# Kernel tuning notes

Measured on AMD Instinct MI355X. Metric: run time of the kernel, lower is better.

Reference implementation:

```python
import jax, jax.numpy as jnp
import numpy as np

B, Wd, C, H, F = 48, 88, 256, 32, 1024
NH_SELF, NH_CROSS = 8, 8


def _ln(x, g, b, eps=1e-5):
    mu = x.mean(-1, keepdims=True)
    var = ((x - mu) ** 2).mean(-1, keepdims=True)
    return (x - mu) / jnp.sqrt(var + eps) * g + b


def setup_inputs() -> dict:
    key = jax.random.key(0)
    ks = jax.random.split(key, 16)
    s = 0.02  # weight init scale
    d = {
        'pooled_features': jax.random.normal(ks[0], (B, Wd, C), jnp.float32),
        'features': jax.random.normal(ks[1], (B, C, H, Wd), jnp.float32),
        'self_pe': jax.random.normal(ks[2], (Wd, C), jnp.float32),
        'cross_pe': jax.random.normal(ks[3], (H, C), jnp.float32),
    }
    # LayerNorm params
    for n in ['ln_qs', 'ln_vs', 'ln_qc', 'ln_kv', 'ln_vc', 'ln_ffn']:
        d[n + '_g'] = jnp.ones((C,), jnp.float32)
        d[n + '_b'] = jnp.zeros((C,), jnp.float32)
    # attention projections (stored [in,out]; y = x @ W + b)
    names = ['Wq_s', 'Wk_s', 'Wv_s', 'Wp_s', 'Wq_c', 'Wk_c', 'Wv_c', 'Wp_c']
    for i, n in enumerate(names):
        d[n] = jax.random.normal(ks[4 + i], (C, C), jnp.float32) * s
    for n in ['bq_s', 'bv_s', 'bp_s', 'bq_c', 'bv_c', 'bp_c']:
        d[n] = jnp.zeros((C,), jnp.float32)
    # FFN
    d['W1'] = jax.random.normal(ks[12], (C, F), jnp.float32) * s
    d['b1'] = jnp.zeros((F,), jnp.float32)
    d['W2'] = jax.random.normal(ks[13], (F, C), jnp.float32) * s
    d['b2'] = jnp.zeros((C,), jnp.float32)
    return d


def reference(pooled_features, features, self_pe, cross_pe,
              ln_qs_g, ln_qs_b, ln_vs_g, ln_vs_b,
              ln_qc_g, ln_qc_b, ln_kv_g, ln_kv_b, ln_vc_g, ln_vc_b,
              ln_ffn_g, ln_ffn_b,
              Wq_s, bq_s, Wk_s, Wv_s, bv_s, Wp_s, bp_s,
              Wq_c, bq_c, Wk_c, Wv_c, bv_c, Wp_c, bp_c,
              W1, b1, W2, b2):
    b, w, c = pooled_features.shape
    h = features.shape[2]
    ds = c // NH_SELF
    dc = c // NH_CROSS

    # ---- cross attention first (op_order='cross_first', with_pe=True) ----
    xq = pooled_features                                  # [B,W,C]
    qn = _ln(xq, ln_qc_g, ln_qc_b)
    kv = jnp.transpose(features, (0, 3, 2, 1))            # [B,W,H,C]
    kn = _ln(kv + cross_pe[None, None], ln_kv_g, ln_kv_b)
    vn = _ln(kv, ln_vc_g, ln_vc_b)
    q = (qn @ Wq_c + bq_c).reshape(b, w, NH_CROSS, dc)    # query len 1 per column
    k = (kn @ Wk_c).reshape(b, w, h, NH_CROSS, dc)
    v = (vn @ Wv_c + bv_c).reshape(b, w, h, NH_CROSS, dc)
    attn = jnp.einsum('bwhd,bwkhd->bwhk', q, k) * (dc ** -0.5)
    attn = jax.nn.softmax(attn, axis=-1)
    out = jnp.einsum('bwhk,bwkhd->bwhd', attn, v).reshape(b, w, c)
    x = out @ Wp_c + bp_c + xq

    # ---- self attention over width tokens ----
    qn = _ln(x + self_pe[None], ln_qs_g, ln_qs_b)
    vn = _ln(x, ln_vs_g, ln_vs_b)
    q = (qn @ Wq_s + bq_s).reshape(b, w, NH_SELF, ds)
    k = (qn @ Wk_s).reshape(b, w, NH_SELF, ds)
    v = (vn @ Wv_s + bv_s).reshape(b, w, NH_SELF, ds)
    attn = jnp.einsum('bnhd,bmhd->bhnm', q, k) * (ds ** -0.5)
    attn = jax.nn.softmax(attn, axis=-1)
    out = jnp.einsum('bhnm,bmhd->bnhd', attn, v).reshape(b, w, c)
    x = out @ Wp_s + bp_s + x

    # ---- FFN (mmcv FFN, num_fcs=2, GELU, identity residual) ----
    hdn = _ln(x, ln_ffn_g, ln_ffn_b)
    hdn = jax.nn.gelu(hdn @ W1 + b1, approximate=False) @ W2 + b2
    return x + hdn
```

## Files before the change

kernel.cpp:

```cpp
#include <hip/hip_runtime.h>
#include <math.h>

#define B_   48
#define W_   88
#define C_   256
#define H_   32
#define F_   1024
#define BW_  (B_ * W_)
#define BWH_ (B_ * W_ * H_)
#define HW_  (H_ * W_)

typedef float  f32x4  __attribute__((ext_vector_type(4)));
typedef __bf16 bf16x8 __attribute__((ext_vector_type(8)));

__device__ __forceinline__ unsigned short f2bf(float f) {
  union { float f; unsigned int u; } v; v.f = f;
  unsigned int r = v.u + 0x7FFFu + ((v.u >> 16) & 1u);
  return (unsigned short)(r >> 16);
}
__device__ __forceinline__ float bf2f(unsigned short h) {
  union { unsigned int u; float f; } v; v.u = ((unsigned int)h) << 16;
  return v.f;
}
__device__ __forceinline__ unsigned int pack2(float a, float b) {
  return (unsigned int)f2bf(a) | ((unsigned int)f2bf(b) << 16);
}

__global__ __launch_bounds__(256) void prep_all(
    const float* __restrict__ Wq_s, const float* __restrict__ Wk_s,
    const float* __restrict__ Wv_s, const float* __restrict__ Wp_s,
    const float* __restrict__ W1, const float* __restrict__ W2,
    const float* __restrict__ Wq_c, const float* __restrict__ Wk_c,
    const float* __restrict__ Wv_c, const float* __restrict__ Wp_c,
    const float* __restrict__ bq_s, const float* __restrict__ bv_s,
    const float* __restrict__ bq_c, const float* __restrict__ bv_c,
    const float* __restrict__ bp_c,
    const float* __restrict__ pooled,
    const float* __restrict__ ln_qc_g, const float* __restrict__ ln_qc_b,
    unsigned short* __restrict__ wqkvs, unsigned short* __restrict__ wps,
    unsigned short* __restrict__ w1t, unsigned short* __restrict__ w2t,
    unsigned short* __restrict__ mqk, unsigned short* __restrict__ mvp,
    float* __restrict__ bqk, float* __restrict__ bvp,
    float* __restrict__ bqkvs, unsigned short* __restrict__ qn_c) {
  __shared__ float smem[256 * 33 + 4 * 33];
  int blk = blockIdx.x, t = threadIdx.x;

  if (blk < 768) {
    const float* src; unsigned short* dst; int Cc, R, tile;
    if (blk < 64)       { src = Wq_s; dst = wqkvs;          Cc = 256;  R = 256;  tile = blk; }
    else if (blk < 128) { src = Wk_s; dst = wqkvs + 65536;  Cc = 256;  R = 256;  tile = blk - 64; }
    else if (blk < 192) { src = Wv_s; dst = wqkvs + 131072; Cc = 256;  R = 256;  tile = blk - 128; }
    else if (blk < 256) { src = Wp_s; dst = wps;            Cc = 256;  R = 256;  tile = blk - 192; }
    else if (blk < 512) { src = W1;   dst = w1t;            Cc = 1024; R = 256;  tile = blk - 256; }
    else                { src = W2;   dst = w2t;            Cc = 256;  R = 1024; tile = blk - 512; }
    int tcn = Cc >> 5;
    int tr = tile / tcn, tc = tile % tcn;
    float (*lds)[33] = (float(*)[33])smem;
    int r = t >> 3, c4 = (t & 7) * 4;
    float4 v = *(const float4*)(src + (size_t)(tr * 32 + r) * Cc + tc * 32 + c4);
    lds[r][c4 + 0] = v.x; lds[r][c4 + 1] = v.y; lds[r][c4 + 2] = v.z; lds[r][c4 + 3] = v.w;
    __syncthreads();
    int rd = t >> 3, cd4 = (t & 7) * 4;
    unsigned int u0 = pack2(lds[cd4 + 0][rd], lds[cd4 + 1][rd]);
    unsigned int u1 = pack2(lds[cd4 + 2][rd], lds[cd4 + 3][rd]);
    uint2 u; u.x = u0; u.y = u1;
    *(uint2*)(dst + (size_t)(tc * 32 + rd) * R + tr * 32 + cd4) = u;
  } else if (blk < 1280) {
    int lb = blk - 768;
    int h = lb >> 6, cb = lb & 63;
    float (*wq)[33] = (float(*)[33])smem;
    float (*wk)[33] = (float(*)[33])(smem + 256 * 33);
#pragma unroll
    for (int p = 0; p < 8; p++) {
      int dp = (t >> 3) + 32 * p, d4 = (t & 7) * 4;
      float4 v = *(const float4*)(Wq_c + (size_t)dp * 256 + 32 * h + d4);
      wq[dp][d4 + 0] = v.x; wq[dp][d4 + 1] = v.y; wq[dp][d4 + 2] = v.z; wq[dp][d4 + 3] = v.w;
    }
    if (t < 128) {
      int c_l = t >> 5, dd = t & 31;
      wk[c_l][dd] = Wk_c[(size_t)(cb * 4 + c_l) * 256 + 32 * h + dd];
    }
    __syncthreads();
    const float scale = 0.17677669529663689f;
    int c_l = t >> 6, ln = t & 63;
    int n = 256 * h + cb * 4 + c_l;
#pragma unroll
    for (int j = 0; j < 4; j++) {
      int dp = ln + 64 * j;
      float acc = 0.f;
#pragma unroll
      for (int dd = 0; dd < 32; dd++) acc += wq[dp][dd] * wk[c_l][dd];
      mqk[(size_t)n * 256 + dp] = f2bf(acc * scale);
    }
    if (ln == 0) {
      float bb = 0.f;
#pragma unroll
      for (int dd = 0; dd < 32; dd++) bb += bq_c[32 * h + dd] * wk[c_l][dd];
      bqk[n] = bb * scale;
    }
  } else if (blk < 1792) {
    int lb = blk - 1280;
    int h = lb >> 6, db = lb & 63;
    float (*wv)[33] = (float(*)[33])smem;
    float (*wp)[33] = (float(*)[33])(smem + 256 * 33);
#pragma unroll
    for (int p = 0; p < 8; p++) {
      int c = (t >> 3) + 32 * p, d4 = (t & 7) * 4;
      float4 v = *(const float4*)(Wv_c + (size_t)c * 256 + 32 * h + d4);
      wv[c][d4 + 0] = v.x; wv[c][d4 + 1] = v.y; wv[c][d4 + 2] = v.z; wv[c][d4 + 3] = v.w;
    }
    if (t < 128) {
      int d_l = t >> 5, dd = t & 31;
      wp[d_l][dd] = Wp_c[(size_t)(32 * h + dd) * 256 + db * 4 + d_l];
    }
    __syncthreads();
    int d_l = t >> 6, ln = t & 63;
    int d = db * 4 + d_l;
#pragma unroll
    for (int j = 0; j < 4; j++) {
      int c = ln + 64 * j;
      float acc = 0.f;
#pragma unroll
      for (int dd = 0; dd < 32; dd++) acc += wv[c][dd] * wp[d_l][dd];
      mvp[(size_t)d * 2048 + 256 * h + c] = f2bf(acc);
    }
  } else if (blk == 1792) {
    float acc = bp_c[t];
    for (int dp = 0; dp < 256; dp++) acc += bv_c[dp] * Wp_c[(size_t)dp * 256 + t];
    bvp[t] = acc;
    bqkvs[t] = bq_s[t]; bqkvs[256 + t] = 0.f; bqkvs[512 + t] = bv_s[t];
  } else {
    int row = blk - 1793, c = t;
    float v = pooled[(size_t)row * C_ + c];
    float s1 = v, s2 = v * v;
#pragma unroll
    for (int m = 32; m > 0; m >>= 1) {
      s1 += __shfl_xor(s1, m, 64); s2 += __shfl_xor(s2, m, 64);
    }
    float* red = smem;
    int wave = c >> 6;
    if ((c & 63) == 0) { red[wave] = s1; red[4 + wave] = s2; }
    __syncthreads();
    s1 = red[0] + red[1] + red[2] + red[3];
    s2 = red[4] + red[5] + red[6] + red[7];
    float mu = s1 * (1.f / C_);
    float rs = rsqrtf(s2 * (1.f / C_) - mu * mu + 1e-5f);
    qn_c[(size_t)row * C_ + c] = f2bf((v - mu) * rs * ln_qc_g[c] + ln_qc_b[c]);
  }
}

__global__ __launch_bounds__(256) void ln_transpose4(
    const float* __restrict__ features, const float* __restrict__ cross_pe,
    const float* __restrict__ g_kv, const float* __restrict__ b_kv,
    const float* __restrict__ g_vc, const float* __restrict__ b_vc,
    unsigned short* __restrict__ kn, unsigned short* __restrict__ vn) {
  int b   = blockIdx.x / 176;
  int tl  = blockIdx.x % 176;
  int hw0 = tl * 16;
  __shared__ float tileT[256][17];
  int t = threadIdx.x;
  {
    int a  = (t & 3) * 4;
    int cc = t >> 2;
    const float* fb = features + (size_t)b * C_ * HW_ + hw0;
#pragma unroll
    for (int p = 0; p < 4; p++) {
      int c = cc + p * 64;
      float4 v = *(const float4*)(fb + (size_t)c * HW_ + a);
      tileT[c][a + 0] = v.x; tileT[c][a + 1] = v.y;
      tileT[c][a + 2] = v.z; tileT[c][a + 3] = v.w;
    }
  }
  __syncthreads();
  int row = t >> 4, ln = t & 15;
  int hw = hw0 + row;
  int hh = hw / 88, ww = hw - hh * 88;
  const float* per = cross_pe + hh * 256;
  float vreg[16], preg[16];
  float s1 = 0, s2 = 0, p1 = 0, p2 = 0;
#pragma unroll
  for (int j = 0; j < 4; j++) {
    int c0 = 4 * ln + 64 * j;
    float4 pv = *(const float4*)(per + c0);
    float pa[4] = {pv.x, pv.y, pv.z, pv.w};
#pragma unroll
    for (int i = 0; i < 4; i++) {
      float v  = tileT[c0 + i][row];
      float vp = v + pa[i];
      vreg[4 * j + i] = v; preg[4 * j + i] = pa[i];
      s1 += v;  s2 += v * v;
      p1 += vp; p2 += vp * vp;
    }
  }
#pragma unroll
  for (int m = 1; m < 16; m <<= 1) {
    s1 += __shfl_xor(s1, m, 16); s2 += __shfl_xor(s2, m, 16);
    p1 += __shfl_xor(p1, m, 16); p2 += __shfl_xor(p2, m, 16);
  }
  float mu  = s1 * (1.f / 256.f);
  float rs  = rsqrtf(s2 * (1.f / 256.f) - mu * mu + 1e-5f);
  float muk = p1 * (1.f / 256.f);
  float rsk = rsqrtf(p2 * (1.f / 256.f) - muk * muk + 1e-5f);
  size_t ro = ((size_t)b * 88 + ww) * 32 + hh;
  unsigned short* vrow = vn + ro * 256;
  unsigned short* krow = kn + ro * 256;
#pragma unroll
  for (int j = 0; j < 4; j++) {
    int c0 = 4 * ln + 64 * j;
    float4 gv = *(const float4*)(g_vc + c0);
    float4 bv = *(const float4*)(b_vc + c0);
    float4 gk = *(const float4*)(g_kv + c0);
    float4 bk = *(const float4*)(b_kv + c0);
    float gva[4] = {gv.x, gv.y, gv.z, gv.w}, bva[4] = {bv.x, bv.y, bv.z, bv.w};
    float gka[4] = {gk.x, gk.y, gk.z, gk.w}, bka[4] = {bk.x, bk.y, bk.z, bk.w};
    float ov[4], ok[4];
#pragma unroll
    for (int i = 0; i < 4; i++) {
      float v = vreg[4 * j + i], p = preg[4 * j + i];
      ov[i] = (v - mu) * rs * gva[i] + bva[i];
      ok[i] = (v + p - muk) * rsk * gka[i] + bka[i];
    }
    uint2 uv, uk;
    uv.x = pack2(ov[0], ov[1]); uv.y = pack2(ov[2], ov[3]);
    uk.x = pack2(ok[0], ok[1]); uk.y = pack2(ok[2], ok[3]);
    *(uint2*)(vrow + c0) = uv;
    *(uint2*)(krow + c0) = uk;
  }
}

__global__ __launch_bounds__(256) void ln_rows(
    const float* __restrict__ x,
    const float* __restrict__ g, const float* __restrict__ bta,
    unsigned short* __restrict__ out) {
  int row = blockIdx.x, c = threadIdx.x;
  float v = x[(size_t)row * C_ + c];
  float s1 = v, s2 = v * v;
#pragma unroll
  for (int m = 32; m > 0; m >>= 1) {
    s1 += __shfl_xor(s1, m, 64);
    s2 += __shfl_xor(s2, m, 64);
  }
  __shared__ float red[8];
  int wave = c >> 6;
  if ((c & 63) == 0) { red[wave] = s1; red[4 + wave] = s2; }
  __syncthreads();
  s1 = red[0] + red[1] + red[2] + red[3];
  s2 = red[4] + red[5] + red[6] + red[7];
  float mu = s1 * (1.f / C_);
  float rs = rsqrtf(s2 * (1.f / C_) - mu * mu + 1e-5f);
  out[(size_t)row * C_ + c] = f2bf((v - mu) * rs * g[c] + bta[c]);
}

__global__ __launch_bounds__(256) void ln_dual(
    const float* __restrict__ x, const float* __restrict__ pe,
    const float* __restrict__ g1, const float* __restrict__ b1a,
    const float* __restrict__ g2, const float* __restrict__ b2a,
    unsigned short* __restrict__ out1, unsigned short* __restrict__ out2) {
  int row = blockIdx.x, c = threadIdx.x;
  float v = x[(size_t)row * C_ + c];
  float vp = v + pe[(size_t)(row % 88) * C_ + c];
  float s1 = v, s2 = v * v, t1 = vp, t2 = vp * vp;
#pragma unroll
  for (int m = 32; m > 0; m >>= 1) {
    s1 += __shfl_xor(s1, m, 64); s2 += __shfl_xor(s2, m, 64);
    t1 += __shfl_xor(t1, m, 64); t2 += __shfl_xor(t2, m, 64);
  }
  __shared__ float red[16];
  int wave = c >> 6;
  if ((c & 63) == 0) {
    red[wave] = s1; red[4 + wave] = s2; red[8 + wave] = t1; red[12 + wave] = t2;
  }
  __syncthreads();
  s1 = red[0] + red[1] + red[2] + red[3];
  s2 = red[4] + red[5] + red[6] + red[7];
  t1 = red[8] + red[9] + red[10] + red[11];
  t2 = red[12] + red[13] + red[14] + red[15];
  float mu = s1 * (1.f / C_), rs = rsqrtf(s2 * (1.f / C_) - mu * mu + 1e-5f);
  float mup = t1 * (1.f / C_), rsp = rsqrtf(t2 * (1.f / C_) - mup * mup + 1e-5f);
  out1[(size_t)row * C_ + c] = f2bf((vp - mup) * rsp * g1[c] + b1a[c]);
  out2[(size_t)row * C_ + c] = f2bf((v - mu) * rs * g2[c] + b2a[c]);
}

__global__ __launch_bounds__(256) void gemm_bt(
    const unsigned short* __restrict__ A, const unsigned short* __restrict__ Bt,
    int M, int N, int K,
    const float* __restrict__ bias, const float* __restrict__ resid,
    float* __restrict__ outF, unsigned short* __restrict__ outB, int act_gelu) {
  __shared__ __attribute__((aligned(16))) unsigned short As[64][32];
  __shared__ __attribute__((aligned(16))) unsigned short Bs[64][32];
  const int tiles_n = N >> 6;
  const int bm = blockIdx.x / tiles_n;
  const int bn = blockIdx.x % tiles_n;
  const int tid = threadIdx.x;
  const int wave = tid >> 6, lane = tid & 63;
  const int quad = lane >> 4, lr = lane & 15;
  const int wm = (wave >> 1) << 5, wn = (wave & 1) << 5;
  const int lrow = tid >> 2;
  const int lcol = (tid & 3) << 3;
  const size_t a_base = (size_t)(bm * 64 + lrow) * K + lcol;
  const size_t b_base = (size_t)(bn * 64 + lrow) * K + lcol;
  f32x4 acc[2][2] = {};
  uint4 areg = *(const uint4*)(A + a_base);
  uint4 breg = *(const uint4*)(Bt + b_base);
  for (int k0 = 0; k0 < K; k0 += 32) {
    *(uint4*)&As[lrow][lcol] = areg;
    *(uint4*)&Bs[lrow][lcol] = breg;
    __syncthreads();
    if (k0 + 32 < K) {
      areg = *(const uint4*)(A + a_base + k0 + 32);
      breg = *(const uint4*)(Bt + b_base + k0 + 32);
    }
    bf16x8 af0 = *(const bf16x8*)&As[wm + lr][quad << 3];
    bf16x8 af1 = *(const bf16x8*)&As[wm + 16 + lr][quad << 3];
    bf16x8 bf0 = *(const bf16x8*)&Bs[wn + lr][quad << 3];
    bf16x8 bf1 = *(const bf16x8*)&Bs[wn + 16 + lr][quad << 3];
    acc[0][0] = __builtin_amdgcn_mfma_f32_16x16x32_bf16(af0, bf0, acc[0][0], 0, 0, 0);
    acc[0][1] = __builtin_amdgcn_mfma_f32_16x16x32_bf16(af0, bf1, acc[0][1], 0, 0, 0);
    acc[1][0] = __builtin_amdgcn_mfma_f32_16x16x32_bf16(af1, bf0, acc[1][0], 0, 0, 0);
    acc[1][1] = __builtin_amdgcn_mfma_f32_16x16x32_bf16(af1, bf1, acc[1][1], 0, 0, 0);
    __syncthreads();
  }
#pragma unroll
  for (int i = 0; i < 2; i++)
#pragma unroll
    for (int j = 0; j < 2; j++)
#pragma unroll
      for (int rr = 0; rr < 4; rr++) {
        int row = bm * 64 + wm + i * 16 + quad * 4 + rr;
        int col = bn * 64 + wn + j * 16 + lr;
        float val = acc[i][j][rr];
        if (bias) val += bias[col];
        if (act_gelu) val = 0.5f * val * (1.f + erff(val * 0.70710678118654752f));
        if (resid) val += resid[(size_t)row * N + col];
        if (outF) outF[(size_t)row * N + col] = val;
        else outB[(size_t)row * N + col] = f2bf(val);
      }
}

__global__ __launch_bounds__(256) void gemm_bt_st(
    const unsigned short* __restrict__ A, const unsigned short* __restrict__ Bt,
    int M, int N, int K, int ldc,
    const float* __restrict__ bias, float* __restrict__ outF) {
  __shared__ __attribute__((aligned(16))) unsigned short As[64][32];
  __shared__ __attribute__((aligned(16))) unsigned short Bs[64][32];
  const int tiles_n = N >> 6;
  const int bm = blockIdx.x / tiles_n;
  const int bn = blockIdx.x % tiles_n;
  const int tid = threadIdx.x;
  const int wave = tid >> 6, lane = tid & 63;
  const int quad = lane >> 4, lr = lane & 15;
  const int wm = (wave >> 1) << 5, wn = (wave & 1) << 5;
  const int lrow = tid >> 2;
  const int lcol = (tid & 3) << 3;
  const size_t a_base = (size_t)(bm * 64 + lrow) * K + lcol;
  const size_t b_base = (size_t)(bn * 64 + lrow) * K + lcol;
  f32x4 acc[2][2] = {};
  uint4 areg = *(const uint4*)(A + a_base);
  uint4 breg = *(const uint4*)(Bt + b_base);
  for (int k0 = 0; k0 < K; k0 += 32) {
    *(uint4*)&As[lrow][lcol] = areg;
    *(uint4*)&Bs[lrow][lcol] = breg;
    __syncthreads();
    if (k0 + 32 < K) {
      areg = *(const uint4*)(A + a_base + k0 + 32);
      breg = *(const uint4*)(Bt + b_base + k0 + 32);
    }
    bf16x8 af0 = *(const bf16x8*)&As[wm + lr][quad << 3];
    bf16x8 af1 = *(const bf16x8*)&As[wm + 16 + lr][quad << 3];
    bf16x8 bf0 = *(const bf16x8*)&Bs[wn + lr][quad << 3];
    bf16x8 bf1 = *(const bf16x8*)&Bs[wn + 16 + lr][quad << 3];
    acc[0][0] = __builtin_amdgcn_mfma_f32_16x16x32_bf16(af0, bf0, acc[0][0], 0, 0, 0);
    acc[0][1] = __builtin_amdgcn_mfma_f32_16x16x32_bf16(af0, bf1, acc[0][1], 0, 0, 0);
    acc[1][0] = __builtin_amdgcn_mfma_f32_16x16x32_bf16(af1, bf0, acc[1][0], 0, 0, 0);
    acc[1][1] = __builtin_amdgcn_mfma_f32_16x16x32_bf16(af1, bf1, acc[1][1], 0, 0, 0);
    __syncthreads();
  }
#pragma unroll
  for (int i = 0; i < 2; i++)
#pragma unroll
    for (int j = 0; j < 2; j++)
#pragma unroll
      for (int rr = 0; rr < 4; rr++) {
        int row = bm * 64 + wm + i * 16 + quad * 4 + rr;
        int col = bn * 64 + wn + j * 16 + lr;
        outF[(size_t)row * ldc + col] = acc[i][j][rr] + bias[col];
      }
}

#define KSTR 264
__global__ __launch_bounds__(256) void cross_attn2(
    const unsigned short* __restrict__ qt_g,
    const unsigned short* __restrict__ kn, const unsigned short* __restrict__ vn,
    unsigned short* __restrict__ ctx_g) {
  int bw = blockIdx.x;
  int tid = threadIdx.x;
  __shared__ __attribute__((aligned(16))) unsigned short qtl[8][KSTR];
  __shared__ __attribute__((aligned(16))) unsigned short knl[32][KSTR];
  __shared__ __attribute__((aligned(16))) unsigned short vnl[32][KSTR];
  __shared__ float s_sc[32 * 9];
  __shared__ float ps[8 * 36];
  __shared__ __attribute__((aligned(16))) unsigned short ctxl[2048];
  {
    uint4 qv = *(const uint4*)(qt_g + (size_t)bw * 2048 + tid * 8);
    int h = tid >> 5, c0 = (tid & 31) * 8;
    *(uint4*)&qtl[h][c0] = qv;
    int j = tid >> 3, cs = (tid & 7) * 32;
    const unsigned short* kr = kn + ((size_t)bw * 32 + j) * 256 + cs;
    const unsigned short* vr = vn + ((size_t)bw * 32 + j) * 256 + cs;
#pragma unroll
    for (int k = 0; k < 4; k++) {
      *(uint4*)&knl[j][cs + k * 8] = *(const uint4*)(kr + k * 8);
      *(uint4*)&vnl[j][cs + k * 8] = *(const uint4*)(vr + k * 8);
    }
  }
  __syncthreads();
  {
    int j = tid >> 3, h = tid & 7;
    float acc = 0.f;
#pragma unroll
    for (int c8 = 0; c8 < 32; c8++) {
      bf16x8 kk = *(const bf16x8*)&knl[j][c8 * 8];
      bf16x8 qq = *(const bf16x8*)&qtl[h][c8 * 8];
#pragma unroll
      for (int i = 0; i < 8; i++) acc += (float)qq[i] * (float)kk[i];
    }
    s_sc[j * 9 + h] = acc;
  }
  __syncthreads();
  {
    int h = tid >> 5, j = tid & 31;
    float s = s_sc[j * 9 + h];
    float mx = s;
#pragma unroll
    for (int m = 16; m > 0; m >>= 1) mx = fmaxf(mx, __shfl_xor(mx, m, 32));
    float e = __expf(s - mx);
    float sum = e;
#pragma unroll
    for (int m = 16; m > 0; m >>= 1) sum += __shfl_xor(sum, m, 32);
    ps[h * 36 + j] = e / sum;
  }
  __syncthreads();
  {
    int h = tid & 7, c0 = (tid >> 3) * 8;
    float acc[8];
#pragma unroll
    for (int i = 0; i < 8; i++) acc[i] = 0.f;
#pragma unroll 8
    for (int j = 0; j < 32; j++) {
      float p = ps[h * 36 + j];
      bf16x8 vv = *(const bf16x8*)&vnl[j][c0];
#pragma unroll
      for (int i = 0; i < 8; i++) acc[i] += p * (float)vv[i];
    }
    unsigned short pk[8];
#pragma unroll
    for (int i = 0; i < 8; i++) pk[i] = f2bf(acc[i]);
    *(uint4*)&ctxl[h * 256 + c0] = *(uint4*)pk;
  }
  __syncthreads();
  *(uint4*)(ctx_g + (size_t)bw * 2048 + tid * 8) = *(const uint4*)&ctxl[tid * 8];
}

__global__ __launch_bounds__(192) void self_attn3(
    const float* __restrict__ qkv, unsigned short* __restrict__ out) {
  int b = blockIdx.x >> 3;
  int h = blockIdx.x & 7;
  int t = threadIdx.x;
  __shared__ float kl[88][33];
  __shared__ float vl[88][33];
  for (int i = t; i < 704; i += 192) {
    int m = i >> 3, d4 = (i & 7) << 2;
    float4 kv4 = *(const float4*)(qkv + (size_t)(b * 88 + m) * 768 + 256 + h * 32 + d4);
    float4 vv4 = *(const float4*)(qkv + (size_t)(b * 88 + m) * 768 + 512 + h * 32 + d4);
    kl[m][d4 + 0] = kv4.x; kl[m][d4 + 1] = kv4.y; kl[m][d4 + 2] = kv4.z; kl[m][d4 + 3] = kv4.w;
    vl[m][d4 + 0] = vv4.x; vl[m][d4 + 1] = vv4.y; vl[m][d4 + 2] = vv4.z; vl[m][d4 + 3] = vv4.w;
  }
  __syncthreads();
  int r = t >> 1, dh = t & 1;
  if (r < 88) {
    const float* qrow = qkv + (size_t)(b * 88 + r) * 768 + h * 32;
    float qr[32];
#pragma unroll
    for (int g = 0; g < 8; g++) {
      float4 q4 = *(const float4*)(qrow + g * 4);
      qr[g * 4 + 0] = q4.x; qr[g * 4 + 1] = q4.y; qr[g * 4 + 2] = q4.z; qr[g * 4 + 3] = q4.w;
    }
    float sreg[44];
    float mx = -1e30f;
    int m0 = dh * 44;
    for (int mi = 0; mi < 44; mi++) {
      const float* krow = kl[m0 + mi];
      float s = 0.f;
#pragma unroll
      for (int d = 0; d < 32; d++) s += qr[d] * krow[d];
      s *= 0.17677669529663689f;
      sreg[mi] = s;
      mx = fmaxf(mx, s);
    }
    mx = fmaxf(mx, __shfl_xor(mx, 1, 64));
    float sum = 0.f;
    for (int mi = 0; mi < 44; mi++) { float e = __expf(sreg[mi] - mx); sreg[mi] = e; sum += e; }
    sum += __shfl_xor(sum, 1, 64);
    float inv = 1.f / sum;
    float o[32];
#pragma unroll
    for (int d = 0; d < 32; d++) o[d] = 0.f;
    for (int mi = 0; mi < 44; mi++) {
      float p = sreg[mi] * inv;
      const float* vrow = vl[m0 + mi];
#pragma unroll
      for (int d = 0; d < 32; d++) o[d] += p * vrow[d];
    }
#pragma unroll
    for (int d = 0; d < 32; d++) o[d] += __shfl_xor(o[d], 1, 64);
    unsigned short* orow = out + (size_t)(b * 88 + r) * 256 + h * 32 + dh * 16;
    uint4 u0, u1;
    int d0 = dh * 16;
    u0.x = pack2(o[d0 + 0], o[d0 + 1]);  u0.y = pack2(o[d0 + 2], o[d0 + 3]);
    u0.z = pack2(o[d0 + 4], o[d0 + 5]);  u0.w = pack2(o[d0 + 6], o[d0 + 7]);
    u1.x = pack2(o[d0 + 8], o[d0 + 9]);  u1.y = pack2(o[d0 + 10], o[d0 + 11]);
    u1.z = pack2(o[d0 + 12], o[d0 + 13]); u1.w = pack2(o[d0 + 14], o[d0 + 15]);
    *(uint4*)(orow) = u0;
    *(uint4*)(orow + 8) = u1;
  }
}

extern "C" void kernel_launch(void* const* d_in, const int* in_sizes, int n_in,
                              void* d_out, int out_size, void* d_ws, size_t ws_size,
                              hipStream_t stream) {
  (void)in_sizes; (void)n_in; (void)out_size; (void)ws_size;
  const float* pooled   = (const float*)d_in[0];
  const float* features = (const float*)d_in[1];
  const float* self_pe  = (const float*)d_in[2];
  const float* cross_pe = (const float*)d_in[3];
  const float* ln_qs_g = (const float*)d_in[4],  *ln_qs_b = (const float*)d_in[5];
  const float* ln_vs_g = (const float*)d_in[6],  *ln_vs_b = (const float*)d_in[7];
  const float* ln_qc_g = (const float*)d_in[8],  *ln_qc_b = (const float*)d_in[9];
  const float* ln_kv_g = (const float*)d_in[10], *ln_kv_b = (const float*)d_in[11];
  const float* ln_vc_g = (const float*)d_in[12], *ln_vc_b = (const float*)d_in[13];
  const float* ln_ffn_g = (const float*)d_in[14], *ln_ffn_b = (const float*)d_in[15];
  const float* Wq_s = (const float*)d_in[16], *Wk_s = (const float*)d_in[17];
  const float* Wv_s = (const float*)d_in[18], *Wp_s = (const float*)d_in[19];
  const float* Wq_c = (const float*)d_in[20], *Wk_c = (const float*)d_in[21];
  const float* Wv_c = (const float*)d_in[22], *Wp_c = (const float*)d_in[23];
  const float* bq_s = (const float*)d_in[24], *bv_s = (const float*)d_in[25];
  const float* bp_s = (const float*)d_in[26], *bq_c = (const float*)d_in[27];
  const float* bv_c = (const float*)d_in[28], *bp_c = (const float*)d_in[29];
  const float* W1 = (const float*)d_in[30], *b1 = (const float*)d_in[31];
  const float* W2 = (const float*)d_in[32], *b2 = (const float*)d_in[33];
  float* outp = (float*)d_out;
  char* ws = (char*)d_ws;

  size_t off = 0;
  auto alloc = [&](size_t bytes) { size_t o = off; off = (off + bytes + 255) & ~(size_t)255; return o; };
  const size_t big = (size_t)BWH_ * C_ * 2;
  size_t KN  = alloc(big);
  size_t VN  = alloc(big);
  size_t QT  = alloc((size_t)BW_ * 2048 * 2);
  size_t CTX = alloc((size_t)BW_ * 2048 * 2);
  size_t MQK = alloc((size_t)2048 * 256 * 2);
  size_t MVP = alloc((size_t)256 * 2048 * 2);
  size_t BQK = alloc(2048 * 4);
  size_t BVP = alloc(256 * 4);
  size_t WQKVS = alloc((size_t)768 * 256 * 2);
  size_t BQKVS = alloc(768 * 4);
  size_t WPS = alloc(65536 * 2);
  size_t W1T = alloc(262144 * 2), W2T = alloc(262144 * 2);
  size_t QN_C = alloc((size_t)BW_ * C_ * 2);
  size_t offp = KN;
  auto allocP = [&](size_t bytes) { size_t o = offp; offp = (offp + bytes + 255) & ~(size_t)255; return o; };
  size_t X1    = allocP((size_t)BW_ * C_ * 4);
  size_t QN_S  = allocP((size_t)BW_ * C_ * 2);
  size_t VN_S  = allocP((size_t)BW_ * C_ * 2);
  size_t QKV_S = allocP((size_t)BW_ * 768 * 4);
  size_t S_O   = allocP((size_t)BW_ * C_ * 2);
  size_t X2    = allocP((size_t)BW_ * C_ * 4);
  size_t FFN   = allocP((size_t)BW_ * C_ * 2);
  size_t H1    = allocP((size_t)BW_ * F_ * 2);

  unsigned short* kn   = (unsigned short*)(ws + KN);
  unsigned short* vn   = (unsigned short*)(ws + VN);
  unsigned short* qt   = (unsigned short*)(ws + QT);
  unsigned short* ctx  = (unsigned short*)(ws + CTX);
  unsigned short* mqk  = (unsigned short*)(ws + MQK);
  unsigned short* mvp  = (unsigned short*)(ws + MVP);
  float* bqk = (float*)(ws + BQK);
  float* bvp = (float*)(ws + BVP);
  unsigned short* wqkvs = (unsigned short*)(ws + WQKVS);
  float* bqkvs = (float*)(ws + BQKVS);
  unsigned short* wps = (unsigned short*)(ws + WPS);
  unsigned short* w1t = (unsigned short*)(ws + W1T), *w2t = (unsigned short*)(ws + W2T);
  unsigned short* qn_c = (unsigned short*)(ws + QN_C);
  float*          x1   = (float*)(ws + X1);
  unsigned short* qn_s = (unsigned short*)(ws + QN_S);
  unsigned short* vn_s = (unsigned short*)(ws + VN_S);
  float* qkv_s = (float*)(ws + QKV_S);
  unsigned short* s_o  = (unsigned short*)(ws + S_O);
  float*          x2   = (float*)(ws + X2);
  unsigned short* ffn_n = (unsigned short*)(ws + FFN);
  unsigned short* h1    = (unsigned short*)(ws + H1);

  prep_all<<<6017, 256, 0, stream>>>(
      Wq_s, Wk_s, Wv_s, Wp_s, W1, W2, Wq_c, Wk_c, Wv_c, Wp_c,
      bq_s, bv_s, bq_c, bv_c, bp_c, pooled, ln_qc_g, ln_qc_b,
      wqkvs, wps, w1t, w2t, mqk, mvp, bqk, bvp, bqkvs, qn_c);

  ln_transpose4<<<B_ * 176, 256, 0, stream>>>(features, cross_pe,
      ln_kv_g, ln_kv_b, ln_vc_g, ln_vc_b, kn, vn);

  gemm_bt<<<(BW_ / 64) * (2048 / 64), 256, 0, stream>>>(qn_c, mqk, BW_, 2048, 256,
      bqk, nullptr, nullptr, qt, 0);

  cross_attn2<<<BW_, 256, 0, stream>>>(qt, kn, vn, ctx);

  gemm_bt<<<(BW_ / 64) * (C_ / 64), 256, 0, stream>>>(ctx, mvp, BW_, C_, 2048,
      bvp, pooled, x1, nullptr, 0);

  ln_dual<<<BW_, 256, 0, stream>>>(x1, self_pe, ln_qs_g, ln_qs_b,
                                   ln_vs_g, ln_vs_b, qn_s, vn_s);

  gemm_bt_st<<<(BW_ / 64) * (512 / 64), 256, 0, stream>>>(qn_s, wqkvs, BW_, 512, 256,
      768, bqkvs, qkv_s);
  gemm_bt_st<<<(BW_ / 64) * (256 / 64), 256, 0, stream>>>(vn_s, wqkvs + 131072, BW_, 256, 256,
      768, bqkvs + 512, qkv_s + 512);

  self_attn3<<<B_ * 8, 192, 0, stream>>>(qkv_s, s_o);

  gemm_bt<<<(BW_ / 64) * (C_ / 64), 256, 0, stream>>>(s_o, wps, BW_, C_, C_,
      bp_s, x1, x2, nullptr, 0);

  ln_rows<<<BW_, 256, 0, stream>>>(x2, ln_ffn_g, ln_ffn_b, ffn_n);
  gemm_bt<<<(BW_ / 64) * (F_ / 64), 256, 0, stream>>>(ffn_n, w1t, BW_, F_, C_,
      b1, nullptr, nullptr, h1, 1);
  gemm_bt<<<(BW_ / 64) * (C_ / 64), 256, 0, stream>>>(h1, w2t, BW_, C_, F_,
      b2, x2, outp, nullptr, 0);
}
```

Before: 532.7 us.

## Fold key/value LayerNorm algebraically into cross-attention, skip materialized KN/VN

Stops writing the normalized, transposed K and V tensors (two large bf16 buffers). Instead it reads features directly in a channel-chunked layout. Cross-attention scores come from partial dot products plus per-row statistics, with the LayerNorm applied afterwards through mean/rstd corrections. Context vectors are built from softmax weights pre-scaled by rstd, minus a mean term. This drops a large write and read of KN/VN. In exchange it reads features twice, writes fp32 partial buffers, and adds a split-reduction kernel.

New measurement: 900.1 us. +69.0%, slower.

```diff
diff --git a/kernel.cpp b/kernel.cpp
--- a/kernel.cpp
+++ b/kernel.cpp
@@ -35,13 +35,14 @@
     const float* __restrict__ bq_s, const float* __restrict__ bv_s,
     const float* __restrict__ bq_c, const float* __restrict__ bv_c,
     const float* __restrict__ bp_c,
-    const float* __restrict__ pooled,
+    const float* __restrict__ pooled, const float* __restrict__ cross_pe,
     const float* __restrict__ ln_qc_g, const float* __restrict__ ln_qc_b,
     unsigned short* __restrict__ wqkvs, unsigned short* __restrict__ wps,
     unsigned short* __restrict__ w1t, unsigned short* __restrict__ w2t,
     unsigned short* __restrict__ mqk, unsigned short* __restrict__ mvp,
     float* __restrict__ bqk, float* __restrict__ bvp,
-    float* __restrict__ bqkvs, unsigned short* __restrict__ qn_c) {
+    float* __restrict__ bqkvs, float* __restrict__ spe,
+    unsigned short* __restrict__ qn_c) {
   __shared__ float smem[256 * 33 + 4 * 33];
   int blk = blockIdx.x, t = threadIdx.x;
 
@@ -61,9 +62,9 @@
     lds[r][c4 + 0] = v.x; lds[r][c4 + 1] = v.y; lds[r][c4 + 2] = v.z; lds[r][c4 + 3] = v.w;
     __syncthreads();
     int rd = t >> 3, cd4 = (t & 7) * 4;
-    unsigned int u0 = pack2(lds[cd4 + 0][rd], lds[cd4 + 1][rd]);
-    unsigned int u1 = pack2(lds[cd4 + 2][rd], lds[cd4 + 3][rd]);
-    uint2 u; u.x = u0; u.y = u1;
+    uint2 u;
+    u.x = pack2(lds[cd4 + 0][rd], lds[cd4 + 1][rd]);
+    u.y = pack2(lds[cd4 + 2][rd], lds[cd4 + 3][rd]);
     *(uint2*)(dst + (size_t)(tc * 32 + rd) * R + tr * 32 + cd4) = u;
   } else if (blk < 1280) {
     int lb = blk - 768;
@@ -129,8 +130,22 @@
     for (int dp = 0; dp < 256; dp++) acc += bv_c[dp] * Wp_c[(size_t)dp * 256 + t];
     bvp[t] = acc;
     bqkvs[t] = bq_s[t]; bqkvs[256 + t] = 0.f; bqkvs[512 + t] = bv_s[t];
+  } else if (blk == 1793) {
+    int j = t >> 3, cp = t & 7;
+    float sp = 0.f, sp2 = 0.f;
+    for (int i = 0; i < 32; i++) {
+      float v = cross_pe[j * 256 + cp * 32 + i];
+      sp += v; sp2 += v * v;
+    }
+    smem[j * 8 + cp] = sp; smem[256 + j * 8 + cp] = sp2;
+    __syncthreads();
+    if (t < 32) {
+      float a = 0.f, a2 = 0.f;
+      for (int i = 0; i < 8; i++) { a += smem[t * 8 + i]; a2 += smem[256 + t * 8 + i]; }
+      spe[t] = a; spe[32 + t] = a2;
+    }
   } else {
-    int row = blk - 1793, c = t;
+    int row = blk - 1794, c = t;
     float v = pooled[(size_t)row * C_ + c];
     float s1 = v, s2 = v * v;
 #pragma unroll
@@ -149,83 +164,208 @@
   }
 }
 
-__global__ __launch_bounds__(256) void ln_transpose4(
-    const float* __restrict__ features, const float* __restrict__ cross_pe,
-    const float* __restrict__ g_kv, const float* __restrict__ b_kv,
-    const float* __restrict__ g_vc, const float* __restrict__ b_vc,
-    unsigned short* __restrict__ kn, unsigned short* __restrict__ vn) {
-  int b   = blockIdx.x / 176;
-  int tl  = blockIdx.x % 176;
-  int hw0 = tl * 16;
-  __shared__ float tileT[256][17];
-  int t = threadIdx.x;
+__global__ __launch_bounds__(704) void xattn_score(
+    const float* __restrict__ features, const unsigned short* __restrict__ qt,
+    const float* __restrict__ gk, const float* __restrict__ cross_pe,
+    float* __restrict__ part1, float* __restrict__ pstat) {
+  int b = blockIdx.x >> 4, ch = blockIdx.x & 15, c0 = ch * 16;
+  __shared__ unsigned short kvl[2][16 * 8 * 88];
+  __shared__ float pel[32][16];
+  int t = threadIdx.x, w = t >> 3, head = t & 7;
+  if (t < 512) {
+    int j = t >> 4, c = t & 15;
+    pel[j][c] = cross_pe[j * 256 + c0 + c];
+  }
+  float gq[16];
   {
-    int a  = (t & 3) * 4;
-    int cc = t >> 2;
-    const float* fb = features + (size_t)b * C_ * HW_ + hw0;
-#pragma unroll
-    for (int p = 0; p < 4; p++) {
-      int c = cc + p * 64;
-      float4 v = *(const float4*)(fb + (size_t)c * HW_ + a);
-      tileT[c][a + 0] = v.x; tileT[c][a + 1] = v.y;
-      tileT[c][a + 2] = v.z; tileT[c][a + 3] = v.w;
-    }
-  }
+    const unsigned short* qrow = qt + (size_t)(b * 88 + w) * 2048 + head * 256 + c0;
+#pragma unroll
+    for (int c = 0; c < 16; c++) gq[c] = gk[c0 + c] * bf2f(qrow[c]);
+  }
+  float a1[32];
+#pragma unroll
+  for (int i = 0; i < 32; i++) a1[i] = 0.f;
+
+  const float* fbase = features + (size_t)(b * 256 + c0) * HW_;
+  float4 rg[4];
+  int iA[4];
+  auto loadq = [&](int q) {
+#pragma unroll
+    for (int k = 0; k < 4; k++) {
+      int p4 = t + k * 704;
+      int c = p4 / 176, r = p4 - c * 176;
+      int j8 = r / 22, w4 = (r - j8 * 22) * 4;
+      iA[k] = (c * 8 + j8) * 88 + w4;
+      rg[k] = *(const float4*)(fbase + (size_t)c * HW_ + (q * 8 + j8) * 88 + w4);
+    }
+  };
+  auto storeq = [&](int buf) {
+#pragma unroll
+    for (int k = 0; k < 4; k++) {
+      uint2 u;
+      u.x = pack2(rg[k].x, rg[k].y);
+      u.y = pack2(rg[k].z, rg[k].w);
+      *(uint2*)&kvl[buf][iA[k]] = u;
+    }
+  };
+  loadq(0); storeq(0);
   __syncthreads();
-  int row = t >> 4, ln = t & 15;
-  int hw = hw0 + row;
-  int hh = hw / 88, ww = hw - hh * 88;
-  const float* per = cross_pe + hh * 256;
-  float vreg[16], preg[16];
-  float s1 = 0, s2 = 0, p1 = 0, p2 = 0;
-#pragma unroll
-  for (int j = 0; j < 4; j++) {
-    int c0 = 4 * ln + 64 * j;
-    float4 pv = *(const float4*)(per + c0);
-    float pa[4] = {pv.x, pv.y, pv.z, pv.w};
-#pragma unroll
-    for (int i = 0; i < 4; i++) {
-      float v  = tileT[c0 + i][row];
-      float vp = v + pa[i];
-      vreg[4 * j + i] = v; preg[4 * j + i] = pa[i];
-      s1 += v;  s2 += v * v;
-      p1 += vp; p2 += vp * vp;
-    }
-  }
-#pragma unroll
-  for (int m = 1; m < 16; m <<= 1) {
-    s1 += __shfl_xor(s1, m, 16); s2 += __shfl_xor(s2, m, 16);
-    p1 += __shfl_xor(p1, m, 16); p2 += __shfl_xor(p2, m, 16);
-  }
+#pragma unroll
+  for (int q = 0; q < 4; q++) {
+    int cur = q & 1, jb = q * 8;
+    if (q < 3) loadq(q + 1);
+    const unsigned short* kb = kvl[cur];
+#pragma unroll
+    for (int c = 0; c < 16; c++) {
+      float g = gq[c];
+      const unsigned short* row = kb + c * 8 * 88 + w;
+#pragma unroll
+      for (int j8 = 0; j8 < 8; j8++)
+        a1[jb + j8] += g * (bf2f(row[j8 * 88]) + pel[jb + j8][c]);
+    }
+    {
+      int jg = jb + head;
+      float s1 = 0.f, s2 = 0.f, cr = 0.f;
+#pragma unroll
+      for (int c = 0; c < 16; c++) {
+        float v = bf2f(kb[(c * 8 + head) * 88 + w]);
+        s1 += v; s2 += v * v; cr += v * pel[jg][c];
+      }
+      size_t sb = (size_t)(b * 16 + ch) * 3 * 2816 + jg * 88 + w;
+      pstat[sb] = s1; pstat[sb + 2816] = s2; pstat[sb + 5632] = cr;
+    }
+    if (q < 3) storeq(cur ^ 1);
+    __syncthreads();
+  }
+  float* dst = part1 + (size_t)((b * 16 + ch) * 88 + w) * 256 + head * 32;
+#pragma unroll
+  for (int i = 0; i < 32; i += 4) {
+    float4 v; v.x = a1[i]; v.y = a1[i + 1]; v.z = a1[i + 2]; v.w = a1[i + 3];
+    *(float4*)(dst + i) = v;
+  }
+}
+
+__global__ __launch_bounds__(256) void xattn_sm(
+    const float* __restrict__ part1, const float* __restrict__ pstat,
+    const unsigned short* __restrict__ qt, const float* __restrict__ spe,
+    const float* __restrict__ gk, const float* __restrict__ bk,
+    float* __restrict__ pr, float* __restrict__ s2a) {
+  int bw = blockIdx.x, b = bw / 88, w = bw - b * 88;
+  int t = threadIdx.x, head = t >> 5, j = t & 31;
+  __shared__ float statl[3][32];
+  float a1 = 0.f;
+  for (int ch = 0; ch < 16; ch++)
+    a1 += part1[(size_t)((b * 16 + ch) * 88 + w) * 256 + t];
+  if (t < 96) {
+    int s = t >> 5, jj = t & 31;
+    float v = 0.f;
+    for (int ch = 0; ch < 16; ch++)
+      v += pstat[(size_t)(b * 16 + ch) * 3 * 2816 + s * 2816 + jj * 88 + w];
+    statl[s][jj] = v;
+  }
+  __syncthreads();
+  float s1 = statl[0][j], s2v = statl[1][j], cr = statl[2][j];
   float mu  = s1 * (1.f / 256.f);
-  float rs  = rsqrtf(s2 * (1.f / 256.f) - mu * mu + 1e-5f);
-  float muk = p1 * (1.f / 256.f);
-  float rsk = rsqrtf(p2 * (1.f / 256.f) - muk * muk + 1e-5f);
-  size_t ro = ((size_t)b * 88 + ww) * 32 + hh;
-  unsigned short* vrow = vn + ro * 256;
-  unsigned short* krow = kn + ro * 256;
-#pragma unroll
-  for (int j = 0; j < 4; j++) {
-    int c0 = 4 * ln + 64 * j;
-    float4 gv = *(const float4*)(g_vc + c0);
-    float4 bv = *(const float4*)(b_vc + c0);
-    float4 gk = *(const float4*)(g_kv + c0);
-    float4 bk = *(const float4*)(b_kv + c0);
-    float gva[4] = {gv.x, gv.y, gv.z, gv.w}, bva[4] = {bv.x, bv.y, bv.z, bv.w};
-    float gka[4] = {gk.x, gk.y, gk.z, gk.w}, bka[4] = {bk.x, bk.y, bk.z, bk.w};
-    float ov[4], ok[4];
-#pragma unroll
-    for (int i = 0; i < 4; i++) {
-      float v = vreg[4 * j + i], p = preg[4 * j + i];
-      ov[i] = (v - mu) * rs * gva[i] + bva[i];
-      ok[i] = (v + p - muk) * rsk * gka[i] + bka[i];
-    }
-    uint2 uv, uk;
-    uv.x = pack2(ov[0], ov[1]); uv.y = pack2(ov[2], ov[3]);
-    uk.x = pack2(ok[0], ok[1]); uk.y = pack2(ok[2], ok[3]);
-    *(uint2*)(vrow + c0) = uv;
-    *(uint2*)(krow + c0) = uk;
-  }
+  float rs  = rsqrtf(s2v * (1.f / 256.f) - mu * mu + 1e-5f);
+  float muk = (s1 + spe[j]) * (1.f / 256.f);
+  float rsk = rsqrtf((s2v + 2.f * cr + spe[32 + j]) * (1.f / 256.f) - muk * muk + 1e-5f);
+  float a3 = 0.f, a4 = 0.f;
+  {
+    const unsigned short* qrow = qt + (size_t)bw * 2048 + head * 256 + j * 8;
+#pragma unroll
+    for (int i = 0; i < 8; i++) {
+      int c = j * 8 + i;
+      float qv = bf2f(qrow[i]);
+      a3 += bk[c] * qv; a4 += gk[c] * qv;
+    }
+  }
+#pragma unroll
+  for (int m = 16; m > 0; m >>= 1) { a3 += __shfl_xor(a3, m, 32); a4 += __shfl_xor(a4, m, 32); }
+  float s = rsk * a1 + a3 - muk * rsk * a4;
+  float mx = s;
+#pragma unroll
+  for (int m = 16; m > 0; m >>= 1) mx = fmaxf(mx, __shfl_xor(mx, m, 32));
+  float e = __expf(s - mx);
+  float sum = e;
+#pragma unroll
+  for (int m = 16; m > 0; m >>= 1) sum += __shfl_xor(sum, m, 32);
+  float p = e / sum;
+  pr[((size_t)bw * 8 + head) * 32 + j] = p * rs;
+  float sp = p * rs * mu;
+#pragma unroll
+  for (int m = 16; m > 0; m >>= 1) sp += __shfl_xor(sp, m, 32);
+  if (j == 0) s2a[(size_t)bw * 8 + head] = sp;
+}
+
+__global__ __launch_bounds__(704) void xattn_ctx(
+    const float* __restrict__ features, const float* __restrict__ pr,
+    const float* __restrict__ s2a, const float* __restrict__ gv,
+    const float* __restrict__ bvv, unsigned short* __restrict__ ctx) {
+  int b = blockIdx.x >> 4, ch = blockIdx.x & 15, c0 = ch * 16;
+  __shared__ unsigned short kvl[2][16 * 8 * 88];
+  int t = threadIdx.x, w = t >> 3, head = t & 7;
+  float prr[32];
+  {
+    const float* p = pr + ((size_t)(b * 88 + w) * 8 + head) * 32;
+#pragma unroll
+    for (int i = 0; i < 32; i += 4) {
+      float4 v = *(const float4*)(p + i);
+      prr[i] = v.x; prr[i + 1] = v.y; prr[i + 2] = v.z; prr[i + 3] = v.w;
+    }
+  }
+  float S2 = s2a[(size_t)(b * 88 + w) * 8 + head];
+  float U[16];
+#pragma unroll
+  for (int i = 0; i < 16; i++) U[i] = 0.f;
+
+  const float* fbase = features + (size_t)(b * 256 + c0) * HW_;
+  float4 rg[4];
+  int iA[4];
+  auto loadq = [&](int q) {
+#pragma unroll
+    for (int k = 0; k < 4; k++) {
+      int p4 = t + k * 704;
+      int c = p4 / 176, r = p4 - c * 176;
+      int j8 = r / 22, w4 = (r - j8 * 22) * 4;
+      iA[k] = (c * 8 + j8) * 88 + w4;
+      rg[k] = *(const float4*)(fbase + (size_t)c * HW_ + (q * 8 + j8) * 88 + w4);
+    }
+  };
+  auto storeq = [&](int buf) {
+#pragma unroll
+    for (int k = 0; k < 4; k++) {
+      uint2 u;
+      u.x = pack2(rg[k].x, rg[k].y);
+      u.y = pack2(rg[k].z, rg[k].w);
+      *(uint2*)&kvl[buf][iA[k]] = u;
+    }
+  };
+  loadq(0); storeq(0);
+  __syncthreads();
+#pragma unroll
+  for (int q = 0; q < 4; q++) {
+    int cur = q & 1, jb = q * 8;
+    if (q < 3) loadq(q + 1);
+    const unsigned short* kb = kvl[cur];
+#pragma unroll
+    for (int c = 0; c < 16; c++) {
+      const unsigned short* row = kb + c * 8 * 88 + w;
+      float acc = U[c];
+#pragma unroll
+      for (int j8 = 0; j8 < 8; j8++)
+        acc += prr[jb + j8] * bf2f(row[j8 * 88]);
+      U[c] = acc;
+    }
+    if (q < 3) storeq(cur ^ 1);
+    __syncthreads();
+  }
+  unsigned short* orow = ctx + (size_t)(b * 88 + w) * 2048 + head * 256 + c0;
+  unsigned short pk[16];
+#pragma unroll
+  for (int i = 0; i < 16; i++)
+    pk[i] = f2bf(gv[c0 + i] * (U[i] - S2) + bvv[c0 + i]);
+  *(uint4*)(orow) = *(uint4*)pk;
+  *(uint4*)(orow + 8) = *(uint4*)(pk + 8);
 }
 
 __global__ __launch_bounds__(256) void ln_rows(
@@ -385,80 +525,6 @@
         int col = bn * 64 + wn + j * 16 + lr;
         outF[(size_t)row * ldc + col] = acc[i][j][rr] + bias[col];
       }
-}
-
-#define KSTR 264
-__global__ __launch_bounds__(256) void cross_attn2(
-    const unsigned short* __restrict__ qt_g,
-    const unsigned short* __restrict__ kn, const unsigned short* __restrict__ vn,
-    unsigned short* __restrict__ ctx_g) {
-  int bw = blockIdx.x;
-  int tid = threadIdx.x;
-  __shared__ __attribute__((aligned(16))) unsigned short qtl[8][KSTR];
-  __shared__ __attribute__((aligned(16))) unsigned short knl[32][KSTR];
-  __shared__ __attribute__((aligned(16))) unsigned short vnl[32][KSTR];
-  __shared__ float s_sc[32 * 9];
-  __shared__ float ps[8 * 36];
-  __shared__ __attribute__((aligned(16))) unsigned short ctxl[2048];
-  {
-    uint4 qv = *(const uint4*)(qt_g + (size_t)bw * 2048 + tid * 8);
-    int h = tid >> 5, c0 = (tid & 31) * 8;
-    *(uint4*)&qtl[h][c0] = qv;
-    int j = tid >> 3, cs = (tid & 7) * 32;
-    const unsigned short* kr = kn + ((size_t)bw * 32 + j) * 256 + cs;
-    const unsigned short* vr = vn + ((size_t)bw * 32 + j) * 256 + cs;
-#pragma unroll
-    for (int k = 0; k < 4; k++) {
-      *(uint4*)&knl[j][cs + k * 8] = *(const uint4*)(kr + k * 8);
-      *(uint4*)&vnl[j][cs + k * 8] = *(const uint4*)(vr + k * 8);
-    }
-  }
-  __syncthreads();
-  {
-    int j = tid >> 3, h = tid & 7;
-    float acc = 0.f;
-#pragma unroll
-    for (int c8 = 0; c8 < 32; c8++) {
-      bf16x8 kk = *(const bf16x8*)&knl[j][c8 * 8];
-      bf16x8 qq = *(const bf16x8*)&qtl[h][c8 * 8];
-#pragma unroll
-      for (int i = 0; i < 8; i++) acc += (float)qq[i] * (float)kk[i];
-    }
-    s_sc[j * 9 + h] = acc;
-  }
-  __syncthreads();
-  {
-    int h = tid >> 5, j = tid & 31;
-    float s = s_sc[j * 9 + h];
-    float mx = s;
-#pragma unroll
-    for (int m = 16; m > 0; m >>= 1) mx = fmaxf(mx, __shfl_xor(mx, m, 32));
-    float e = __expf(s - mx);
-    float sum = e;
-#pragma unroll
-    for (int m = 16; m > 0; m >>= 1) sum += __shfl_xor(sum, m, 32);
-    ps[h * 36 + j] = e / sum;
-  }
-  __syncthreads();
-  {
-    int h = tid & 7, c0 = (tid >> 3) * 8;
-    float acc[8];
-#pragma unroll
-    for (int i = 0; i < 8; i++) acc[i] = 0.f;
-#pragma unroll 8
-    for (int j = 0; j < 32; j++) {
-      float p = ps[h * 36 + j];
-      bf16x8 vv = *(const bf16x8*)&vnl[j][c0];
-#pragma unroll
-      for (int i = 0; i < 8; i++) acc[i] += p * (float)vv[i];
-    }
-    unsigned short pk[8];
-#pragma unroll
-    for (int i = 0; i < 8; i++) pk[i] = f2bf(acc[i]);
-    *(uint4*)&ctxl[h * 256 + c0] = *(uint4*)pk;
-  }
-  __syncthreads();
-  *(uint4*)(ctx_g + (size_t)bw * 2048 + tid * 8) = *(const uint4*)&ctxl[tid * 8];
 }
 
 __global__ __launch_bounds__(192) void self_attn3(
@@ -553,21 +619,23 @@
 
   size_t off = 0;
   auto alloc = [&](size_t bytes) { size_t o = off; off = (off + bytes + 255) & ~(size_t)255; return o; };
-  const size_t big = (size_t)BWH_ * C_ * 2;
-  size_t KN  = alloc(big);
-  size_t VN  = alloc(big);
-  size_t QT  = alloc((size_t)BW_ * 2048 * 2);
-  size_t CTX = alloc((size_t)BW_ * 2048 * 2);
-  size_t MQK = alloc((size_t)2048 * 256 * 2);
-  size_t MVP = alloc((size_t)256 * 2048 * 2);
-  size_t BQK = alloc(2048 * 4);
-  size_t BVP = alloc(256 * 4);
+  size_t QT   = alloc((size_t)BW_ * 2048 * 2);
+  size_t CTX  = alloc((size_t)BW_ * 2048 * 2);
+  size_t MQK  = alloc((size_t)2048 * 256 * 2);
+  size_t MVP  = alloc((size_t)256 * 2048 * 2);
+  size_t BQK  = alloc(2048 * 4);
+  size_t BVP  = alloc(256 * 4);
   size_t WQKVS = alloc((size_t)768 * 256 * 2);
   size_t BQKVS = alloc(768 * 4);
   size_t WPS = alloc(65536 * 2);
   size_t W1T = alloc(262144 * 2), W2T = alloc(262144 * 2);
   size_t QN_C = alloc((size_t)BW_ * C_ * 2);
-  size_t offp = KN;
+  size_t SPE  = alloc(64 * 4);
+  size_t PART1 = alloc((size_t)48 * 16 * 88 * 256 * 4);
+  size_t PSTAT = alloc((size_t)48 * 16 * 3 * 2816 * 4);
+  size_t PRB   = alloc((size_t)BW_ * 256 * 4);
+  size_t S2A   = alloc((size_t)BW_ * 8 * 4);
+  size_t offp = PART1;
   auto allocP = [&](size_t bytes) { size_t o = offp; offp = (offp + bytes + 255) & ~(size_t)255; return o; };
   size_t X1    = allocP((size_t)BW_ * C_ * 4);
   size_t QN_S  = allocP((size_t)BW_ * C_ * 2);
@@ -578,9 +646,7 @@
   size_t FFN   = allocP((size_t)BW_ * C_ * 2);
   size_t H1    = allocP((size_t)BW_ * F_ * 2);
 
-  unsigned short* kn   = (unsigned short*)(ws + KN);
-  unsigned short* vn   = (unsigned short*)(ws + VN);
-  unsigned short* qt   = (unsigned short*)(ws + QT);
+  unsigned short* qtp  = (unsigned short*)(ws + QT);
   unsigned short* ctx  = (unsigned short*)(ws + CTX);
   unsigned short* mqk  = (unsigned short*)(ws + MQK);
   unsigned short* mvp  = (unsigned short*)(ws + MVP);
@@ -591,6 +657,11 @@
   unsigned short* wps = (unsigned short*)(ws + WPS);
   unsigned short* w1t = (unsigned short*)(ws + W1T), *w2t = (unsigned short*)(ws + W2T);
   unsigned short* qn_c = (unsigned short*)(ws + QN_C);
+  float* spe   = (float*)(ws + SPE);
+  float* part1 = (float*)(ws + PART1);
+  float* pstat = (float*)(ws + PSTAT);
+  float* prb   = (float*)(ws + PRB);
+  float* s2a   = (float*)(ws + S2A);
   float*          x1   = (float*)(ws + X1);
   unsigned short* qn_s = (unsigned short*)(ws + QN_S);
   unsigned short* vn_s = (unsigned short*)(ws + VN_S);
@@ -600,18 +671,17 @@
   unsigned short* ffn_n = (unsigned short*)(ws + FFN);
   unsigned short* h1    = (unsigned short*)(ws + H1);
 
-  prep_all<<<6017, 256, 0, stream>>>(
+  prep_all<<<6018, 256, 0, stream>>>(
       Wq_s, Wk_s, Wv_s, Wp_s, W1, W2, Wq_c, Wk_c, Wv_c, Wp_c,
-      bq_s, bv_s, bq_c, bv_c, bp_c, pooled, ln_qc_g, ln_qc_b,
-      wqkvs, wps, w1t, w2t, mqk, mvp, bqk, bvp, bqkvs, qn_c);
-
-  ln_transpose4<<<B_ * 176, 256, 0, stream>>>(features, cross_pe,
-      ln_kv_g, ln_kv_b, ln_vc_g, ln_vc_b, kn, vn);
+      bq_s, bv_s, bq_c, bv_c, bp_c, pooled, cross_pe, ln_qc_g, ln_qc_b,
+      wqkvs, wps, w1t, w2t, mqk, mvp, bqk, bvp, bqkvs, spe, qn_c);
 
   gemm_bt<<<(BW_ / 64) * (2048 / 64), 256, 0, stream>>>(qn_c, mqk, BW_, 2048, 256,
-      bqk, nullptr, nullptr, qt, 0);
-
-  cross_attn2<<<BW_, 256, 0, stream>>>(qt, kn, vn, ctx);
+      bqk, nullptr, nullptr, qtp, 0);
+
+  xattn_score<<<768, 704, 0, stream>>>(features, qtp, ln_kv_g, cross_pe, part1, pstat);
+  xattn_sm<<<BW_, 256, 0, stream>>>(part1, pstat, qtp, spe, ln_kv_g, ln_kv_b, prb, s2a);
+  xattn_ctx<<<768, 704, 0, stream>>>(features, prb, s2a, ln_vc_g, ln_vc_b, ctx);
 
   gemm_bt<<<(BW_ / 64) * (C_ / 64), 256, 0, stream>>>(ctx, mvp, BW_, C_, 2048,
       bvp, pooled, x1, nullptr, 0);
```
